# Kernel tuning notes

Measured on AMD Instinct MI355X. Metric: run time of the kernel, lower is better.

Reference implementation:

```python
import jax, jax.numpy as jnp
import numpy as np

L, B, T, D, V = 2, 16, 20, 768, 30000


def setup_inputs() -> dict:
    key = jax.random.key(0)
    k1, k2, k3, k4 = jax.random.split(key, 4)
    answer_embed = jax.random.normal(k1, (L, B, T, D), dtype=jnp.float32)
    vocab_embed = 0.1 * jax.random.normal(k2, (V, D), dtype=jnp.float32)
    # classifier_transform modeled as Linear(D, D): y = x @ W.T + b
    W = jax.random.normal(k3, (D, D), dtype=jnp.float32) * (1.0 / np.sqrt(D))
    b = jax.random.normal(k4, (D,), dtype=jnp.float32) * 0.01
    return {"answer_embed": answer_embed, "vocab_embed": vocab_embed, "W": W, "b": b}


def reference(answer_embed, vocab_embed, W, b):
    # vocab_classifiers: [V, D] after the linear transform
    vocab_classifiers = vocab_embed @ W.T + b
    # Original: broadcast multiply [L,B,T,D,1]*[1,1,1,D,V] then sum over D.
    # Mathematically identical contraction over D -> [L, B, T, V]
    return jnp.einsum('lbtd,vd->lbtv', answer_embed, vocab_classifiers)
```

## Files before the change

### kernel.cpp

```cpp
#include <hip/hip_runtime.h>

#define KDIM 768
#define MANS 640
#define VV   30000
#define NGRP 235
#define NKS  (KDIM / 64)
#define VELEM (VV * KDIM)
#define CVTBLK ((VELEM + 8191) / 8192)
#define A2BLK  ((MANS / 64) * (KDIM / 128))

typedef __attribute__((ext_vector_type(4)))  float  f32x4;
typedef __attribute__((ext_vector_type(16))) float  f32x16;
typedef __attribute__((ext_vector_type(8)))  __bf16 bf16x8;
typedef __attribute__((ext_vector_type(8)))  unsigned short ushort8;

__device__ __forceinline__ unsigned short f2bf(float f) {
    union { __bf16 h; unsigned short u; } t;
    t.h = (__bf16)f;
    return t.u;
}

__device__ __forceinline__ ushort8 cvt8(f32x4 a, f32x4 b) {
    union { bf16x8 h; ushort8 u; } c;
    c.h[0] = (__bf16)a.x; c.h[1] = (__bf16)a.y;
    c.h[2] = (__bf16)a.z; c.h[3] = (__bf16)a.w;
    c.h[4] = (__bf16)b.x; c.h[5] = (__bf16)b.y;
    c.h[6] = (__bf16)b.z; c.h[7] = (__bf16)b.w;
    return c.u;
}

__device__ __forceinline__ void load_lds16(const unsigned short* g, unsigned short* l) {
    __builtin_amdgcn_global_load_lds(
        (__attribute__((address_space(1))) void*)(void*)g,
        (__attribute__((address_space(3))) void*)l,
        16, 0, 0);
}

__device__ __forceinline__ long a2f_off(int m, int n) {
    int mb = m >> 7, wm = (m >> 6) & 1, fm = (m >> 5) & 1, colm = m & 31;
    int kt = n >> 6, g = (n >> 4) & 3, halfb = (n >> 3) & 1, e = n & 7;
    return ((((long)(mb * 12 + kt) * 2 + wm) * 2 + fm) * 4 + g) * 512
         + (halfb * 32 + colm) * 8 + e;
}

__global__ __launch_bounds__(256) void prep_small(
    const float* __restrict__ W, const float* __restrict__ A,
    const float* __restrict__ b, unsigned short* __restrict__ Wt_bf,
    float* __restrict__ cvec)
{
    __shared__ float ts[64][65];
    const int blk = blockIdx.x;
    if (blk < 144) {
        int bx = (blk % 12) * 64, by = (blk / 12) * 64;
        int tx = threadIdx.x & 63, tg = threadIdx.x >> 6;
#pragma unroll
        for (int i = 0; i < 16; ++i) {
            int r = tg * 16 + i;
            ts[r][tx] = W[(long)(by + r) * KDIM + bx + tx];
        }
        __syncthreads();
#pragma unroll
        for (int i = 0; i < 16; ++i) {
            int r = tg * 16 + i;
            Wt_bf[(long)(bx + r) * KDIM + by + tx] = f2bf(ts[tx][r]);
        }
    } else {
        int row  = (blk - 144) * 4 + (threadIdx.x >> 6);
        int lane = threadIdx.x & 63;
        const float* ap = A + (long)row * KDIM;
        float s = 0.f;
#pragma unroll
        for (int i = 0; i < KDIM / 64; ++i) s += ap[i * 64 + lane] * b[i * 64 + lane];
#pragma unroll
        for (int off = 32; off; off >>= 1) s += __shfl_down(s, off, 64);
        if (lane == 0) cvec[row] = s;
    }
}

__global__ __launch_bounds__(256) void gemm_a2(
    const float* __restrict__ Af, const unsigned short* __restrict__ Bp,
    unsigned short* __restrict__ outp,
    const float* __restrict__ vocab, unsigned short* __restrict__ vocab_bf)
{
    if (blockIdx.x >= A2BLK) {
        const long base = (long)(blockIdx.x - A2BLK) * 8192 + (long)threadIdx.x * 8;
#pragma unroll
        for (int p = 0; p < 4; ++p) {
            long idx = base + p * 2048;
            if (idx < VELEM) {
                f32x4 v0 = ((const f32x4*)(vocab + idx))[0];
                f32x4 v1 = ((const f32x4*)(vocab + idx))[1];
                *(ushort8*)(vocab_bf + idx) = cvt8(v0, v1);
            }
        }
        return;
    }

    constexpr int TM = 64, TN = 128;
    __shared__ unsigned short sA[TM * 64];
    __shared__ unsigned short sB[TN * 64];

    const int t    = threadIdx.x;
    const int lane = t & 63;
    const int w    = t >> 6;
    const int wm   = w >> 1;
    const int wn   = w & 1;
    const int half = lane >> 5;
    const int col  = lane & 31;
    const long m0  = (long)(blockIdx.x % (MANS / 64)) * TM;
    const long n0  = (long)(blockIdx.x / (MANS / 64)) * TN;

    f32x16 acc[2];
    acc[0] = (f32x16)(0.f);
    acc[1] = (f32x16)(0.f);

    const float* gaf[2]; int laOff[2];
#pragma unroll
    for (int j = 0; j < 2; ++j) {
        int s   = (j * 4 + w) * 64 + lane;
        int row = s >> 3;
        int c   = (s & 7) ^ (row & 7);
        gaf[j]   = Af + (m0 + row) * KDIM + c * 8;
        laOff[j] = s * 8;
    }
    const unsigned short* gb[4]; unsigned short* lbB[4];
#pragma unroll
    for (int j = 0; j < 4; ++j) {
        int s   = (j * 4 + w) * 64 + lane;
        int row = s >> 3;
        int c   = (s & 7) ^ (row & 7);
        gb[j]  = Bp + (n0 + row) * KDIM + c * 8;
        lbB[j] = &sB[(j * 4 + w) * 64 * 8];
    }

    for (int k0 = 0; k0 < KDIM; k0 += 64) {
#pragma unroll
        for (int j = 0; j < 4; ++j) load_lds16(gb[j] + k0, lbB[j]);
#pragma unroll
        for (int j = 0; j < 2; ++j) {
            f32x4 v0 = ((const f32x4*)(gaf[j] + k0))[0];
            f32x4 v1 = ((const f32x4*)(gaf[j] + k0))[1];
            *(ushort8*)(&sA[0] + laOff[j]) = cvt8(v0, v1);
        }
        __syncthreads();

#pragma unroll
        for (int g = 0; g < 4; ++g) {
            const int cg = g * 2 + half;
            int arow = wm * 32 + col;
            bf16x8 af = *(const bf16x8*)&sA[(arow * 8 + (cg ^ (arow & 7))) * 8];
#pragma unroll
            for (int fn = 0; fn < 2; ++fn) {
                int brow = wn * 64 + fn * 32 + col;
                bf16x8 bfv = *(const bf16x8*)&sB[(brow * 8 + (cg ^ (brow & 7))) * 8];
                acc[fn] = __builtin_amdgcn_mfma_f32_32x32x16_bf16(
                    af, bfv, acc[fn], 0, 0, 0);
            }
        }
        __syncthreads();
    }

#pragma unroll
    for (int fn = 0; fn < 2; ++fn) {
        int n = (int)n0 + wn * 64 + fn * 32 + col;
#pragma unroll
        for (int rg = 0; rg < 16; ++rg) {
            int m = (int)m0 + wm * 32 + (rg & 3) + 8 * (rg >> 2) + 4 * half;
            outp[a2f_off(m, n)] = f2bf(acc[fn][rg]);
        }
    }
}

__global__ __launch_bounds__(256) void gemm_big(
    const unsigned short* __restrict__ A, const unsigned short* __restrict__ Bbf,
    const float* __restrict__ cvec, float* __restrict__ outp)
{
    const int id    = blockIdx.x;
    const int x     = id & 7;
    const int q     = id >> 3;
    const int m_idx = q % 5;
    const int n_grp = (q / 5) * 8 + x;
    if (n_grp >= NGRP) return;

    __shared__ unsigned short sB[2][128 * 64];

    const int t    = threadIdx.x;
    const int lane = t & 63;
    const int w    = t >> 6;
    const int wm   = w >> 1;
    const int wn   = w & 1;
    const int half = lane >> 5;
    const int col  = lane & 31;
    const long n0  = (long)n_grp * 128;

    f32x16 acc[2][2];
#pragma unroll
    for (int i = 0; i < 2; ++i)
#pragma unroll
        for (int j = 0; j < 2; ++j) acc[i][j] = (f32x16)(0.f);

    const unsigned short* aBase = A + (((long)(m_idx * 12) * 2 + wm) * 2) * 4 * 512
                                    + lane * 8;

    const unsigned short* gb[4];
    int lbOff[4];
#pragma unroll
    for (int j = 0; j < 4; ++j) {
        int s   = (j * 4 + w) * 64 + lane;
        int row = s >> 3;
        int c   = (s & 7) ^ (row & 7);
        long grow = n0 + row;
        if (grow > VV - 1) grow = VV - 1;
        gb[j]    = Bbf + grow * KDIM + c * 8;
        lbOff[j] = (j * 4 + w) * 64 * 8;
    }

    auto stage = [&](int kt, int buf) {
        const int o = buf * (128 * 64);
#pragma unroll
        for (int j = 0; j < 4; ++j)
            load_lds16(gb[j] + kt * 64, &sB[0][0] + o + lbOff[j]);
    };

    auto compute = [&](int kt, int buf) {
        const unsigned short* bB = &sB[0][0] + buf * (128 * 64);
        const unsigned short* aK = aBase + (long)kt * 8192;
#pragma unroll
        for (int g = 0; g < 4; ++g) {
            const int cg = g * 2 + half;
            bf16x8 af[2], bfr[2];
#pragma unroll
            for (int fm = 0; fm < 2; ++fm)
                af[fm] = *(const bf16x8*)(aK + fm * 2048 + g * 512);
#pragma unroll
            for (int fn = 0; fn < 2; ++fn) {
                int row = wn * 64 + fn * 32 + col;
                bfr[fn] = *(const bf16x8*)&bB[(row * 8 + (cg ^ (row & 7))) * 8];
            }
#pragma unroll
            for (int fm = 0; fm < 2; ++fm)
#pragma unroll
                for (int fn = 0; fn < 2; ++fn)
                    acc[fm][fn] = __builtin_amdgcn_mfma_f32_32x32x16_bf16(
                        af[fm], bfr[fn], acc[fm][fn], 0, 0, 0);
        }
    };

    stage(0, 0);
    asm volatile("s_waitcnt vmcnt(0)" ::: "memory");
    __builtin_amdgcn_s_barrier();

    int p = 0;
    for (int kt = 0; kt < NKS - 1; ++kt) {
        stage(kt + 1, p ^ 1);
        compute(kt, p);
        asm volatile("s_waitcnt vmcnt(0)" ::: "memory");
        __builtin_amdgcn_s_barrier();
        p ^= 1;
    }
    compute(NKS - 1, p);

    const long m0 = (long)m_idx * 128;
#pragma unroll
    for (int fm = 0; fm < 2; ++fm)
#pragma unroll
        for (int fn = 0; fn < 2; ++fn) {
            long n = n0 + wn * 64 + fn * 32 + col;
            if (n < VV) {
#pragma unroll
                for (int rg = 0; rg < 16; ++rg) {
                    long m = m0 + wm * 64 + fm * 32
                           + (rg & 3) + 8 * (rg >> 2) + 4 * half;
                    outp[m * (long)VV + n] = acc[fm][fn][rg] + cvec[m];
                }
            }
        }
}

extern "C" void kernel_launch(void* const* d_in, const int* in_sizes, int n_in,
                              void* d_out, int out_size, void* d_ws, size_t ws_size,
                              hipStream_t stream) {
    const float* answer = (const float*)d_in[0];
    const float* vocab  = (const float*)d_in[1];
    const float* W      = (const float*)d_in[2];
    const float* bvec   = (const float*)d_in[3];

    char* ws = (char*)d_ws;
    unsigned short* Wt_bf   = (unsigned short*)ws;
    unsigned short* A2F     = (unsigned short*)(ws + 1179648);
    float*          cptr    = (float*)(ws + 1179648 + 983040);
    unsigned short* vocabbf = (unsigned short*)(ws + 2165248);

    prep_small<<<304, 256, 0, stream>>>(W, answer, bvec, Wt_bf, cptr);

    gemm_a2<<<A2BLK + CVTBLK, 256, 0, stream>>>(answer, Wt_bf, A2F, vocab, vocabbf);

    gemm_big<<<1200, 256, 0, stream>>>(A2F, vocabbf, cptr, (float*)d_out);
}
```

Baseline: 222.0 us.

## Pre-swizzle vocab bf16 into MFMA fragment layout and drop LDS staging

The vocab conversion now writes bf16 data directly in the per-lane MFMA fragment order instead of row-major. The big GEMM then loads both operands straight from global memory into registers, which removes the LDS double buffer, the barriers and the swizzle arithmetic. The cost is that B reuse across waves now relies on cache instead of shared memory, there is no explicit prefetch pipeline to hide load latency, and the scattered writes during conversion may coalesce less well.

```diff
diff --git a/kernel.cpp b/kernel.cpp
--- a/kernel.cpp
+++ b/kernel.cpp
@@ -6,7 +6,7 @@
 #define NGRP 235
 #define NKS  (KDIM / 64)
 #define VELEM (VV * KDIM)
-#define CVTBLK ((VELEM + 8191) / 8192)
+#define CVTBLK (VELEM / 8 / 256)
 #define A2BLK  ((MANS / 64) * (KDIM / 128))
 
 typedef __attribute__((ext_vector_type(4)))  float  f32x4;
@@ -42,6 +42,7 @@
     return ((((long)(mb * 12 + kt) * 2 + wm) * 2 + fm) * 4 + g) * 512
          + (halfb * 32 + colm) * 8 + e;
 }
+
 
 __global__ __launch_bounds__(256) void prep_small(
     const float* __restrict__ W, const float* __restrict__ A,
@@ -80,19 +81,18 @@
 __global__ __launch_bounds__(256) void gemm_a2(
     const float* __restrict__ Af, const unsigned short* __restrict__ Bp,
     unsigned short* __restrict__ outp,
-    const float* __restrict__ vocab, unsigned short* __restrict__ vocab_bf)
+    const float* __restrict__ vocab, unsigned short* __restrict__ vocab_vf)
 {
     if (blockIdx.x >= A2BLK) {
-        const long base = (long)(blockIdx.x - A2BLK) * 8192 + (long)threadIdx.x * 8;
-#pragma unroll
-        for (int p = 0; p < 4; ++p) {
-            long idx = base + p * 2048;
-            if (idx < VELEM) {
-                f32x4 v0 = ((const f32x4*)(vocab + idx))[0];
-                f32x4 v1 = ((const f32x4*)(vocab + idx))[1];
-                *(ushort8*)(vocab_bf + idx) = cvt8(v0, v1);
-            }
-        }
+        long id = (long)(blockIdx.x - A2BLK) * 256 + threadIdx.x;
+        int  v  = (int)(id / 96);
+        int  kc = (int)(id % 96);
+        const float* src = vocab + (long)v * KDIM + kc * 8;
+        f32x4 v0 = ((const f32x4*)src)[0], v1 = ((const f32x4*)src)[1];
+        int nt = v >> 5, colv = v & 31;
+        int kt = kc >> 3, g = (kc >> 1) & 3, hb = kc & 1;
+        long off = ((((long)nt * 12 + kt) * 4 + g) * 64 + hb * 32 + colv) * 8;
+        *(ushort8*)(vocab_vf + off) = cvt8(v0, v1);
         return;
     }
 
@@ -172,7 +172,7 @@
 }
 
 __global__ __launch_bounds__(256) void gemm_big(
-    const unsigned short* __restrict__ A, const unsigned short* __restrict__ Bbf,
+    const unsigned short* __restrict__ A, const unsigned short* __restrict__ VF,
     const float* __restrict__ cvec, float* __restrict__ outp)
 {
     const int id    = blockIdx.x;
@@ -182,8 +182,6 @@
     const int n_grp = (q / 5) * 8 + x;
     if (n_grp >= NGRP) return;
 
-    __shared__ unsigned short sB[2][128 * 64];
-
     const int t    = threadIdx.x;
     const int lane = t & 63;
     const int w    = t >> 6;
@@ -199,66 +197,27 @@
 #pragma unroll
         for (int j = 0; j < 2; ++j) acc[i][j] = (f32x16)(0.f);
 
-    const unsigned short* aBase = A + (((long)(m_idx * 12) * 2 + wm) * 2) * 4 * 512
-                                    + lane * 8;
-
-    const unsigned short* gb[4];
-    int lbOff[4];
-#pragma unroll
-    for (int j = 0; j < 4; ++j) {
-        int s   = (j * 4 + w) * 64 + lane;
-        int row = s >> 3;
-        int c   = (s & 7) ^ (row & 7);
-        long grow = n0 + row;
-        if (grow > VV - 1) grow = VV - 1;
-        gb[j]    = Bbf + grow * KDIM + c * 8;
-        lbOff[j] = (j * 4 + w) * 64 * 8;
-    }
-
-    auto stage = [&](int kt, int buf) {
-        const int o = buf * (128 * 64);
-#pragma unroll
-        for (int j = 0; j < 4; ++j)
-            load_lds16(gb[j] + kt * 64, &sB[0][0] + o + lbOff[j]);
-    };
-
-    auto compute = [&](int kt, int buf) {
-        const unsigned short* bB = &sB[0][0] + buf * (128 * 64);
-        const unsigned short* aK = aBase + (long)kt * 8192;
+    const unsigned short* aB = A + ((long)16 * (m_idx * 12) + 8 * wm) * 512
+                                 + lane * 8;
+    const unsigned short* bB = VF + (long)(n_grp * 4 + wn * 2) * 24576
+                                  + lane * 8;
+
+#pragma unroll
+    for (int kt = 0; kt < NKS; ++kt) {
+        const unsigned short* aK = aB + (long)kt * 8192;
+        const unsigned short* bK = bB + (long)kt * 2048;
 #pragma unroll
         for (int g = 0; g < 4; ++g) {
-            const int cg = g * 2 + half;
-            bf16x8 af[2], bfr[2];
-#pragma unroll
-            for (int fm = 0; fm < 2; ++fm)
-                af[fm] = *(const bf16x8*)(aK + fm * 2048 + g * 512);
-#pragma unroll
-            for (int fn = 0; fn < 2; ++fn) {
-                int row = wn * 64 + fn * 32 + col;
-                bfr[fn] = *(const bf16x8*)&bB[(row * 8 + (cg ^ (row & 7))) * 8];
-            }
-#pragma unroll
-            for (int fm = 0; fm < 2; ++fm)
-#pragma unroll
-                for (int fn = 0; fn < 2; ++fn)
-                    acc[fm][fn] = __builtin_amdgcn_mfma_f32_32x32x16_bf16(
-                        af[fm], bfr[fn], acc[fm][fn], 0, 0, 0);
-        }
-    };
-
-    stage(0, 0);
-    asm volatile("s_waitcnt vmcnt(0)" ::: "memory");
-    __builtin_amdgcn_s_barrier();
-
-    int p = 0;
-    for (int kt = 0; kt < NKS - 1; ++kt) {
-        stage(kt + 1, p ^ 1);
-        compute(kt, p);
-        asm volatile("s_waitcnt vmcnt(0)" ::: "memory");
-        __builtin_amdgcn_s_barrier();
-        p ^= 1;
-    }
-    compute(NKS - 1, p);
+            bf16x8 af0 = *(const bf16x8*)(aK + g * 512);
+            bf16x8 af1 = *(const bf16x8*)(aK + 2048 + g * 512);
+            bf16x8 bf0 = *(const bf16x8*)(bK + g * 512);
+            bf16x8 bf1 = *(const bf16x8*)(bK + 24576 + g * 512);
+            acc[0][0] = __builtin_amdgcn_mfma_f32_32x32x16_bf16(af0, bf0, acc[0][0], 0, 0, 0);
+            acc[0][1] = __builtin_amdgcn_mfma_f32_32x32x16_bf16(af0, bf1, acc[0][1], 0, 0, 0);
+            acc[1][0] = __builtin_amdgcn_mfma_f32_32x32x16_bf16(af1, bf0, acc[1][0], 0, 0, 0);
+            acc[1][1] = __builtin_amdgcn_mfma_f32_32x32x16_bf16(af1, bf1, acc[1][1], 0, 0, 0);
+        }
+    }
 
     const long m0 = (long)m_idx * 128;
 #pragma unroll
@@ -289,11 +248,11 @@
     unsigned short* Wt_bf   = (unsigned short*)ws;
     unsigned short* A2F     = (unsigned short*)(ws + 1179648);
     float*          cptr    = (float*)(ws + 1179648 + 983040);
-    unsigned short* vocabbf = (unsigned short*)(ws + 2165248);
+    unsigned short* VF      = (unsigned short*)(ws + 2165248);
 
     prep_small<<<304, 256, 0, stream>>>(W, answer, bvec, Wt_bf, cptr);
 
-    gemm_a2<<<A2BLK + CVTBLK, 256, 0, stream>>>(answer, Wt_bf, A2F, vocab, vocabbf);
-
-    gemm_big<<<1200, 256, 0, stream>>>(A2F, vocabbf, cptr, (float*)d_out);
-}
+    gemm_a2<<<A2BLK + CVTBLK, 256, 0, stream>>>(answer, Wt_bf, A2F, vocab, VF);
+
+    gemm_big<<<1200, 256, 0, stream>>>(A2F, VF, cptr, (float*)d_out);
+}
```

Result: slower. 244.6 us (+10.2%).
